# Optimization experiments

Hardware: AMD Instinct MI355X
Metric: run time of the kernel (lower is better)

Reference implementation:

```python
import jax, jax.numpy as jnp
import numpy as np

S, B, E, H, FFN = 512, 16, 512, 8, 2048
D = E // H
EPS = 1e-6
MAXT = 1.0 - 1e-7


def _norm(x):
    return jnp.sqrt(jnp.sum(x * x, axis=-1, keepdims=True) + 1e-15)


def artanh(x):
    return jnp.arctanh(jnp.clip(x, -MAXT, MAXT))


def expmap0(u):
    n = _norm(u)
    return jnp.tanh(n) * u / n


def logmap0(x):
    n = _norm(x)
    return artanh(n) * x / n


def projx(x):
    n = _norm(x)
    m = 1.0 - 1e-5
    return jnp.where(n > m, x * (m / n), x)


def lambda_x(x):
    return 2.0 / jnp.maximum(1.0 - jnp.sum(x * x, -1, keepdims=True), EPS)


def mobius_add(x, y):
    xy = jnp.sum(x * y, -1, keepdims=True)
    x2 = jnp.sum(x * x, -1, keepdims=True)
    y2 = jnp.sum(y * y, -1, keepdims=True)
    num = (1 + 2 * xy + y2) * x + (1 - x2) * y
    return num / jnp.maximum(1 + 2 * xy + x2 * y2, EPS)


def mobius_scalar_mul(r, x):
    n = _norm(x)
    return jnp.tanh(r * artanh(n)) * x / n


def mobius_matvec(W, x):
    mx = x @ W.T
    nx = _norm(x)
    nmx = _norm(mx)
    res = jnp.tanh(nmx / nx * artanh(nx)) * mx / nmx
    return jnp.where(nmx > 1e-7, res, jnp.zeros_like(mx))


def man_linear(W, b, x):
    return projx(mobius_add(mobius_matvec(W, x), expmap0(b)))


def layernorm(x, g, b):
    mu = x.mean(-1, keepdims=True)
    v = jnp.mean((x - mu) ** 2, -1, keepdims=True)
    return (x - mu) / jnp.sqrt(v + 1e-5) * g + b


def mob_res_midpoint(x1, x2):
    # two_point_mid with w1 = w2 = 1 (Mobius gyromidpoint residual)
    l1, l2 = lambda_x(x1), lambda_x(x2)
    t = (x1 * l1 + x2 * l2) / jnp.maximum(l1 + l2 - 2.0, EPS)
    return mobius_scalar_mul(0.5, t)


def _heads(t):  # [S,B,E] -> [B,H,S,D]
    return t.reshape(S, B, H, D).transpose(1, 2, 0, 3)


def _merge(t):  # [B,H,S,D] -> [S,B,E]
    return t.transpose(2, 0, 1, 3).reshape(S, B, E)


def euclid_expert(x, ln1_g, ln1_b, ln2_g, ln2_b, Wq, bq, Wk, bk, Wv, bv, Wo, bo, W1, b1, W2, b2):
    res = x
    h = layernorm(x, ln1_g, ln1_b)
    q, k, v = _heads(h @ Wq.T + bq), _heads(h @ Wk.T + bk), _heads(h @ Wv.T + bv)
    d2 = jnp.sum(q * q, -1)[..., :, None] + jnp.sum(k * k, -1)[..., None, :] - 2 * jnp.einsum('bhqd,bhkd->bhqk', q, k)
    scores = -jnp.sqrt(jnp.maximum(d2, 0.0) + 1e-12) / np.sqrt(D)
    w = jax.nn.softmax(scores, -1)
    o = _merge(jnp.einsum('bhqk,bhkd->bhqd', w, v))
    x = o @ Wo.T + bo + res
    res = x
    h = layernorm(x, ln2_g, ln2_b)
    h = jax.nn.relu(h @ W1.T + b1)
    h = jax.nn.relu(h @ W2.T + b2)
    return h + res


def hyp_expert(x, ln1_g, ln1_b, ln2_g, ln2_b, Wq, bq, Wk, bk, Wv, bv, Wo, bo, W1, b1, W2, b2):
    res = x
    h = expmap0(layernorm(logmap0(x), ln1_g, ln1_b))
    q = projx(_heads(man_linear(Wq, bq, h)))
    k = projx(_heads(man_linear(Wk, bk, h)))
    v = projx(_heads(man_linear(Wv, bv, h)))
    qq, kk = jnp.sum(q * q, -1), jnp.sum(k * k, -1)
    qk = jnp.einsum('bhqd,bhkd->bhqk', q, k)
    diff2 = jnp.maximum(qq[..., :, None] + kk[..., None, :] - 2 * qk, 0.0)
    den = jnp.maximum(1 - 2 * qk + qq[..., :, None] * kk[..., None, :], EPS)
    dist = 2.0 * artanh(jnp.sqrt(diff2 / den + 1e-15))  # Poincare dist via gyro identity
    w = jax.nn.softmax(-dist / np.sqrt(D), -1)
    lam = lambda_x(v)  # [B,H,S,1]
    num = jnp.einsum('bhqk,bhkd->bhqd', w, v * lam)
    dnm = jnp.maximum(jnp.einsum('bhqk,bhk->bhq', w, lam[..., 0] - 1.0), EPS)[..., None]
    o = projx(mobius_scalar_mul(0.5, num / dnm))  # Mobius gyromidpoint aggregation
    x = projx(man_linear(Wo, bo, projx(_merge(o))))
    x = mob_res_midpoint(x, res)
    res = x
    x = projx(expmap0(layernorm(logmap0(x), ln2_g, ln2_b)))
    x = jax.nn.relu(man_linear(W1, b1, x))
    x = jax.nn.relu(man_linear(W2, b2, x))
    return projx(mob_res_midpoint(x, res))


def setup_inputs():
    key = jax.random.key(0)
    ks = jax.random.split(key, 20)
    x0 = jax.random.normal(ks[0], (S, B, E), jnp.float32)
    x1 = projx(0.05 * jax.random.normal(ks[1], (S, B, E), jnp.float32))
    x = jnp.stack([x0, x1])

    def w(k, *shape):
        return jax.random.normal(k, (2,) + shape, jnp.float32) / np.sqrt(shape[-1])

    return dict(
        x=x,
        ln1_g=jnp.ones((2, E), jnp.float32), ln1_b=jnp.zeros((2, E), jnp.float32),
        ln2_g=jnp.ones((2, E), jnp.float32), ln2_b=jnp.zeros((2, E), jnp.float32),
        Wq=w(ks[2], E, E), bq=0.02 * jax.random.normal(ks[3], (2, E), jnp.float32),
        Wk=w(ks[4], E, E), bk=0.02 * jax.random.normal(ks[5], (2, E), jnp.float32),
        Wv=w(ks[6], E, E), bv=0.02 * jax.random.normal(ks[7], (2, E), jnp.float32),
        Wo=w(ks[8], E, E), bo=0.02 * jax.random.normal(ks[9], (2, E), jnp.float32),
        W1=w(ks[10], FFN, E), b1=0.02 * jax.random.normal(ks[11], (2, FFN), jnp.float32),
        W2=w(ks[12], E, FFN), b2=0.02 * jax.random.normal(ks[13], (2, E), jnp.float32),
    )


def reference(x, ln1_g, ln1_b, ln2_g, ln2_b, Wq, bq, Wk, bk, Wv, bv, Wo, bo, W1, b1, W2, b2):
    args = (ln1_g, ln1_b, ln2_g, ln2_b, Wq, bq, Wk, bk, Wv, bv, Wo, bo, W1, b1, W2, b2)
    out0 = euclid_expert(x[0], *[a[0] for a in args])
    out1 = hyp_expert(x[1], *[a[1] for a in args])
    return jnp.stack([out0, out1])
```

## Files before the change

### kernel.cpp

```cpp
#include <hip/hip_runtime.h>
#include <cstdint>
#include <cstddef>

#define S_ 512
#define B_ 16
#define H_ 8
#define D_ 64
#define E_ 512
#define FFN_ 2048
#define R_ (S_*B_)
#define EPSF 1e-6f
#define PROJ_M 0.99999f

typedef __attribute__((ext_vector_type(8))) short bf16x8;
typedef __attribute__((ext_vector_type(4))) float f32x4;
typedef __attribute__((ext_vector_type(2))) unsigned int u32x2;

__device__ __forceinline__ float bf2f(uint32_t u){
  union{uint32_t i; float f;} c; c.i = u<<16; return c.f;
}
__device__ __forceinline__ uint16_t f2bf(float f){
  union{float f; uint32_t i;} c; c.f = f;
  return (uint16_t)((c.i + 0x7FFFu + ((c.i>>16)&1u))>>16);
}
__device__ __forceinline__ void unpack8(uint4 u, float* f){
  f[0]=bf2f(u.x&0xFFFFu); f[1]=bf2f(u.x>>16);
  f[2]=bf2f(u.y&0xFFFFu); f[3]=bf2f(u.y>>16);
  f[4]=bf2f(u.z&0xFFFFu); f[5]=bf2f(u.z>>16);
  f[6]=bf2f(u.w&0xFFFFu); f[7]=bf2f(u.w>>16);
}
__device__ __forceinline__ uint4 pack8(const float* f){
  uint4 u;
  u.x = (uint32_t)f2bf(f[0]) | ((uint32_t)f2bf(f[1])<<16);
  u.y = (uint32_t)f2bf(f[2]) | ((uint32_t)f2bf(f[3])<<16);
  u.z = (uint32_t)f2bf(f[4]) | ((uint32_t)f2bf(f[5])<<16);
  u.w = (uint32_t)f2bf(f[6]) | ((uint32_t)f2bf(f[7])<<16);
  return u;
}
__device__ __forceinline__ float artanh_c(float x){
  return (x >= 0.99999994f) ? 8.4056215f : atanhf(x);
}
__device__ __forceinline__ float wave_sum(float x){
  #pragma unroll
  for(int o=32;o>=1;o>>=1) x += __shfl_xor(x,o);
  return x;
}
__device__ __forceinline__ float g8sum(float x){
  x += __shfl_xor(x,1); x += __shfl_xor(x,2); x += __shfl_xor(x,4);
  return x;
}
__device__ __forceinline__ float block_sum(float x, float* sb){
  x = wave_sum(x);
  const int w = threadIdx.x >> 6;
  __syncthreads();
  if((threadIdx.x & 63)==0) sb[w] = x;
  __syncthreads();
  return sb[0]+sb[1]+sb[2]+sb[3];
}
__device__ __forceinline__ void gl_lds16(const void* g, void* l){
  __builtin_amdgcn_global_load_lds(
    (const __attribute__((address_space(1))) void*)(uintptr_t)g,
    (__attribute__((address_space(3))) void*)(uint32_t)(uintptr_t)l, 16, 0, 0);
}
__device__ __forceinline__ uint32_t cvtpk(float a, float b){
  uint32_t r;
  asm("v_cvt_pk_bf16_f32 %0, %1, %2" : "=v"(r) : "v"(a), "v"(b));
  return r;
}
template<int OFF>
__device__ __forceinline__ u32x2 trrd(uint32_t addr){
  u32x2 r;
  asm volatile("ds_read_b64_tr_b16 %0, %1 offset:%2" : "=v"(r) : "v"(addr), "n"(OFF));
  return r;
}
__device__ __forceinline__ bf16x8 vcomb(u32x2 a, u32x2 b){
  union{ uint32_t u[4]; bf16x8 v; } c;
  c.u[0]=a[0]; c.u[1]=a[1]; c.u[2]=b[0]; c.u[3]=b[1];
  return c.v;
}

__global__ __launch_bounds__(256) void cvt_all(
  const float* __restrict__ Wq, const float* __restrict__ Wk,
  const float* __restrict__ Wv, const float* __restrict__ Wo,
  const float* __restrict__ W1, const float* __restrict__ W2,
  uint16_t* __restrict__ dst)
{
  int i4 = blockIdx.x*256 + threadIdx.x;
  int e = 0;
  if(i4 >= 786432){ e = 1; i4 -= 786432; }
  const int r = i4;
  const float* s;
  if(r < 65536)        s = Wq + (size_t)(r)*4        + (size_t)e*262144;
  else if(r < 131072)  s = Wk + (size_t)(r-65536)*4  + (size_t)e*262144;
  else if(r < 196608)  s = Wv + (size_t)(r-131072)*4 + (size_t)e*262144;
  else if(r < 262144)  s = Wo + (size_t)(r-196608)*4 + (size_t)e*262144;
  else if(r < 524288)  s = W1 + (size_t)(r-262144)*4 + (size_t)e*1048576;
  else                 s = W2 + (size_t)(r-524288)*4 + (size_t)e*1048576;
  const float4 f = *(const float4*)s;
  uint2 o;
  o.x = (uint32_t)f2bf(f.x) | ((uint32_t)f2bf(f.y)<<16);
  o.y = (uint32_t)f2bf(f.z) | ((uint32_t)f2bf(f.w)<<16);
  *(uint2*)(dst + (size_t)e*3145728 + (size_t)r*4) = o;
}

__global__ __launch_bounds__(256) void expmap_all(
  const float* __restrict__ bq, const float* __restrict__ bk,
  const float* __restrict__ bv, const float* __restrict__ bo,
  const float* __restrict__ b1, const float* __restrict__ b2,
  float* __restrict__ YV)
{
  __shared__ float sb[4];
  const int id = blockIdx.x, t = threadIdx.x;
  const float* src; float* dst; int C;
  if(id==0){ src=bq+E_;   dst=YV+0;    C=E_; }
  else if(id==1){ src=bk+E_;   dst=YV+528;  C=E_; }
  else if(id==2){ src=bv+E_;   dst=YV+1056; C=E_; }
  else if(id==3){ src=bo+E_;   dst=YV+1584; C=E_; }
  else if(id==4){ src=b1+FFN_; dst=YV+2112; C=FFN_; }
  else          { src=b2+E_;   dst=YV+4176; C=E_; }
  const int npc = C >> 8;
  float v[8]; float s2 = 0.f;
  for(int i=0;i<npc;i++){ v[i] = src[t+256*i]; s2 += v[i]*v[i]; }
  s2 = block_sum(s2, sb);
  const float n = sqrtf(s2 + 1e-15f);
  const float th = tanhf(n);
  const float sc = th/n;
  for(int i=0;i<npc;i++) dst[t+256*i] = v[i]*sc;
  if(t==0) dst[C] = th*th;
}

__global__ __launch_bounds__(256) void lnfuseW(const float* __restrict__ x,
  const float* __restrict__ g, const float* __restrict__ b,
  uint16_t* __restrict__ out, float* __restrict__ nout, int do_projx)
{
  const int row = blockIdx.x*4 + (threadIdx.x>>6);
  const int l = threadIdx.x & 63;
  const size_t base = (size_t)row*E_ + l*8;
  const int hyp = (row >= R_);
  const float* gg = g + (hyp? E_ : 0);
  const float* bb = b + (hyp? E_ : 0);
  float v[8];
  *(float4*)(v)   = *(const float4*)(x + base);
  *(float4*)(v+4) = *(const float4*)(x + base + 4);
  float s = 0.f;
  #pragma unroll
  for(int i=0;i<8;i++) s += v[i];
  const float mu = wave_sum(s) * (1.f/E_);
  float q = 0.f;
  #pragma unroll
  for(int i=0;i<8;i++){ v[i] -= mu; q += v[i]*v[i]; }
  const float var = wave_sum(q) * (1.f/E_);
  const float rs = 1.f/sqrtf(var + 1e-5f);
  float gv[8], bvv[8];
  *(float4*)(gv)    = *(const float4*)(gg + l*8);
  *(float4*)(gv+4)  = *(const float4*)(gg + l*8 + 4);
  *(float4*)(bvv)   = *(const float4*)(bb + l*8);
  *(float4*)(bvv+4) = *(const float4*)(bb + l*8 + 4);
  float t[8];
  #pragma unroll
  for(int i=0;i<8;i++) t[i] = v[i]*rs*gv[i] + bvv[i];
  if(hyp){
    float n = 0.f;
    #pragma unroll
    for(int i=0;i<8;i++) n += t[i]*t[i];
    n = wave_sum(n);
    const float n2 = sqrtf(n + 1e-15f);
    const float nh = tanhf(n2);
    float scl = nh/n2;
    float nrm = nh;
    if(do_projx && nrm > PROJ_M){ scl *= PROJ_M/nrm; nrm = PROJ_M; }
    #pragma unroll
    for(int i=0;i<8;i++) t[i] *= scl;
    if(l==0) nout[row - R_] = nrm;
  }
  *(uint4*)(out + base) = pack8(t);
}

__global__ __launch_bounds__(256) void qk_norms(
  const uint16_t* __restrict__ Qb, const uint16_t* __restrict__ Kb,
  float* __restrict__ qn, float* __restrict__ kn)
{
  const int w = threadIdx.x >> 6, l = threadIdx.x & 63;
  const int row = blockIdx.x*4 + w;
  const int s = row >> 4, b = row & 15;
  const size_t base = (size_t)row*E_ + l*8;
  {
    uint4 u = *(const uint4*)(Qb + base);
    float f[8]; unpack8(u, f);
    float ss = 0.f;
    #pragma unroll
    for(int i=0;i<8;i++) ss += f[i]*f[i];
    ss = g8sum(ss);
    if((l&7)==0) qn[((b<<3) + (l>>3))*512 + s] = ss;
  }
  {
    uint4 u = *(const uint4*)(Kb + base);
    float f[8]; unpack8(u, f);
    float ss = 0.f;
    #pragma unroll
    for(int i=0;i<8;i++) ss += f[i]*f[i];
    ss = g8sum(ss);
    if((l&7)==0) kn[((b<<3) + (l>>3))*512 + s] = ss;
  }
}

template<int EPL>
__global__ __launch_bounds__(256) void man_epiW(
  const uint16_t* __restrict__ mxb, const float* __restrict__ nxbuf,
  const float* __restrict__ y, uint16_t* __restrict__ outb,
  float* __restrict__ nout,
  const float* __restrict__ midres, float* __restrict__ midout, int flags)
{
  constexpr int C = EPL*64;
  const int row = blockIdx.x*4 + (threadIdx.x>>6);
  const int l = threadIdx.x & 63;
  const size_t base = (size_t)row*C + l*EPL;
  float v[EPL], yv[EPL];
  #pragma unroll
  for(int i=0;i<EPL/8;i++){
    uint4 u = *(const uint4*)(mxb + base + i*8);
    unpack8(u, v + i*8);
  }
  #pragma unroll
  for(int i=0;i<EPL/4;i++)
    *(float4*)(yv + i*4) = *(const float4*)(y + l*EPL + i*4);
  float s2 = 0.f;
  #pragma unroll
  for(int i=0;i<EPL;i++) s2 += v[i]*v[i];
  s2 = wave_sum(s2);
  const float nmx = sqrtf(s2 + 1e-15f);
  const float nx  = nxbuf[row];
  const float sc  = tanhf(nmx/nx * artanh_c(nx));
  const bool ok   = (nmx > 1e-7f);
  const float fmul = ok ? (sc/nmx) : 0.f;
  const float x2   = ok ? sc*sc : 0.f;
  float xy = 0.f;
  #pragma unroll
  for(int i=0;i<EPL;i++){ v[i] *= fmul; xy += v[i]*yv[i]; }
  xy = wave_sum(xy);
  const float y2 = y[C];
  const float aa = 1.f + 2.f*xy + y2;
  const float bb = 1.f - x2;
  const float iden = 1.f/fmaxf(1.f + 2.f*xy + x2*y2, EPSF);
  const float num2 = aa*aa*x2 + 2.f*aa*bb*xy + bb*bb*y2;
  const float nz = sqrtf(num2*iden*iden + 1e-15f);
  const float ps = (nz > PROJ_M) ? (PROJ_M/nz) : 1.f;
  float nfin = (nz > PROJ_M) ? PROJ_M : nz;
  #pragma unroll
  for(int i=0;i<EPL;i++) v[i] = (aa*v[i] + bb*yv[i]) * iden * ps;
  if(flags & 1){
    float rsu = 0.f;
    #pragma unroll
    for(int i=0;i<EPL;i++){ v[i] = fmaxf(v[i], 0.f); rsu += v[i]*v[i]; }
    rsu = wave_sum(rsu);
    nfin = sqrtf(rsu + 1e-15f);
  }
  if(midres){
    float bv2[EPL];
    #pragma unroll
    for(int i=0;i<EPL/4;i++)
      *(float4*)(bv2 + i*4) = *(const float4*)(midres + base + i*4);
    float pb = 0.f, pab = 0.f;
    #pragma unroll
    for(int i=0;i<EPL;i++){ pb += bv2[i]*bv2[i]; pab += v[i]*bv2[i]; }
    const float sa  = nfin*nfin;
    const float sbb = wave_sum(pb);
    const float sab = wave_sum(pab);
    const float l1 = 2.f/fmaxf(1.f - sa,  EPSF);
    const float l2 = 2.f/fmaxf(1.f - sbb, EPSF);
    const float idn = 1.f/fmaxf(l1 + l2 - 2.f, EPSF);
    const float nt2 = (l1*l1*sa + 2.f*l1*l2*sab + l2*l2*sbb)*idn*idn;
    const float nt = sqrtf(nt2 + 1e-15f);
    const float sfin = tanhf(0.5f*artanh_c(nt));
    float scm = sfin/nt;
    if((flags & 8) && sfin > PROJ_M) scm *= PROJ_M/sfin;
    #pragma unroll
    for(int i=0;i<EPL;i++) midout[base + i] = (v[i]*l1 + bv2[i]*l2)*idn*scm;
  } else {
    #pragma unroll
    for(int i=0;i<EPL/8;i++)
      *(uint4*)(outb + base + i*8) = pack8(v + i*8);
    if(nout && l==0) nout[row] = nfin;
  }
}

__global__ __launch_bounds__(256) void man_epi_qkvW(
  const uint16_t* __restrict__ mxb, const float* __restrict__ nxbuf,
  const float* __restrict__ YV, uint16_t* __restrict__ qkv,
  float* __restrict__ qnG, float* __restrict__ knG, float* __restrict__ lamG)
{
  const int sel = blockIdx.y;
  const int row = blockIdx.x*4 + (threadIdx.x>>6);
  const int l = threadIdx.x & 63;
  const float* y = YV + sel*528;
  const size_t base = (size_t)sel*4194304 + (size_t)row*512 + l*8;
  float v[8], yv[8];
  {
    uint4 u = *(const uint4*)(mxb + base);
    unpack8(u, v);
  }
  *(float4*)(yv)   = *(const float4*)(y + l*8);
  *(float4*)(yv+4) = *(const float4*)(y + l*8 + 4);
  float s2 = 0.f;
  #pragma unroll
  for(int i=0;i<8;i++) s2 += v[i]*v[i];
  s2 = wave_sum(s2);
  const float nmx = sqrtf(s2 + 1e-15f);
  const float nx  = nxbuf[row];
  const float sc  = tanhf(nmx/nx * artanh_c(nx));
  const bool ok   = (nmx > 1e-7f);
  const float fmul = ok ? (sc/nmx) : 0.f;
  const float x2   = ok ? sc*sc : 0.f;
  float xy = 0.f;
  #pragma unroll
  for(int i=0;i<8;i++){ v[i] *= fmul; xy += v[i]*yv[i]; }
  xy = wave_sum(xy);
  const float y2 = y[512];
  const float aa = 1.f + 2.f*xy + y2;
  const float bb = 1.f - x2;
  const float iden = 1.f/fmaxf(1.f + 2.f*xy + x2*y2, EPSF);
  const float num2 = aa*aa*x2 + 2.f*aa*bb*xy + bb*bb*y2;
  const float nz = sqrtf(num2*iden*iden + 1e-15f);
  const float ps = (nz > PROJ_M) ? (PROJ_M/nz) : 1.f;
  #pragma unroll
  for(int i=0;i<8;i++) v[i] = (aa*v[i] + bb*yv[i]) * iden * ps;
  float hs = 0.f;
  #pragma unroll
  for(int i=0;i<8;i++) hs += v[i]*v[i];
  hs = g8sum(hs);
  float nh = sqrtf(hs + 1e-15f);
  float phs = 1.f;
  if(nh > PROJ_M){ phs = PROJ_M/nh; nh = PROJ_M; }
  #pragma unroll
  for(int i=0;i<8;i++) v[i] *= phs;
  const float nh2 = nh*nh;
  const float lam = 2.f/fmaxf(1.f - nh2, EPSF);
  if(sel==2){
    #pragma unroll
    for(int i=0;i<8;i++) v[i] *= lam;
  }
  if((l & 7) == 0){
    const int s = row >> 4, b2 = row & 15;
    const int idx = ((b2<<3) + (l>>3))*512 + s;
    if(sel==0) qnG[idx] = nh2;
    else if(sel==1) knG[idx] = nh2;
    else lamG[idx] = lam;
  }
  *(uint4*)(qkv + base) = pack8(v);
}

__global__ __launch_bounds__(256) void o_finishW(const uint16_t* __restrict__ op,
  uint16_t* __restrict__ outb, float* __restrict__ nout)
{
  const int row = blockIdx.x*4 + (threadIdx.x>>6);
  const int l = threadIdx.x & 63;
  const size_t base = (size_t)row*E_ + l*8;
  float v[8];
  {
    uint4 u = *(const uint4*)(op + base);
    unpack8(u, v);
  }
  float hs = 0.f;
  #pragma unroll
  for(int i=0;i<8;i++) hs += v[i]*v[i];
  hs = g8sum(hs);
  const float ns = sqrtf(hs + 1e-15f);
  const float tt = tanhf(0.5f*artanh_c(ns));
  float scv = tt/ns;
  float sn = tt;
  if(sn > PROJ_M){ scv *= PROJ_M/sn; sn = PROJ_M; }
  float tot = 0.f;
  #pragma unroll
  for(int i=0;i<8;i++){ v[i] *= scv; tot += v[i]*v[i]; }
  tot = wave_sum(tot);
  const float n = sqrtf(tot + 1e-15f);
  float nf = n;
  if(n > PROJ_M){
    const float s = PROJ_M/n;
    #pragma unroll
    for(int i=0;i<8;i++) v[i] *= s;
    nf = PROJ_M;
  }
  *(uint4*)(outb + base) = pack8(v);
  if(l==0) nout[row] = nf;
}

__global__ __launch_bounds__(256) void gemmF(
    const uint16_t* __restrict__ A,
    const uint16_t* __restrict__ Bw0, const uint16_t* __restrict__ Bw1,
    int msplit, int N, int K, int mode0, int mode1,
    const float* __restrict__ bQ, const float* __restrict__ bK,
    const float* __restrict__ bV, const float* __restrict__ res0,
    float* __restrict__ outf0,
    uint16_t* __restrict__ outb0, uint16_t* __restrict__ outb1)
{
  __shared__ __align__(16) char AsB[2][16384];
  __shared__ __align__(16) char BsB[2][16384];
  const int gx = gridDim.x;
  int lid = blockIdx.x + gx*blockIdx.y;
  {
    const int nwg = gx*gridDim.y;
    const int cpx = nwg >> 3;
    lid = (lid & 7)*cpx + (lid >> 3);
  }
  const int m0 = (lid/gx)*128;
  const int n0 = (lid%gx)*128;
  const int e  = (m0 >= msplit);
  const uint16_t* Bw = e ? Bw1 : Bw0;
  uint16_t* ob = e ? outb1 : outb0;
  const int mode = e ? mode1 : mode0;
  const int mloc0 = m0 - (e ? msplit : 0);

  const int tid = threadIdx.x;
  const int l = tid & 63, w = tid >> 6;
  const int wm = w >> 1, wn = w & 1;
  const int lr = l & 15, g = l >> 4;
  const int lr3 = l >> 3, lc = l & 7;
  const int c8s = lc ^ lr3;
  const int swq = (lr & 7) << 4;

  const uint16_t* aSrc = A  + (size_t)(m0 + lr3)*K + c8s*8;
  const uint16_t* bSrc = Bw + (size_t)(n0 + lr3)*K + c8s*8;

  f32x4 acc[4][4];
  #pragma unroll
  for(int i=0;i<4;i++)
    #pragma unroll
    for(int j=0;j<4;j++) acc[i][j] = (f32x4){0.f,0.f,0.f,0.f};

  const int nk = K >> 6;
  #pragma unroll
  for(int c=0;c<4;c++){
    const int ci = w*4 + c;
    gl_lds16(aSrc + (size_t)(ci*8)*K, AsB[0] + ci*1024);
    gl_lds16(bSrc + (size_t)(ci*8)*K, BsB[0] + ci*1024);
  }
  for(int ks=0; ks<nk; ks++){
    __syncthreads();
    if(ks+1 < nk){
      const int k0 = (ks+1) << 6;
      #pragma unroll
      for(int c=0;c<4;c++){
        const int ci = w*4 + c;
        gl_lds16(aSrc + (size_t)(ci*8)*K + k0, AsB[(ks+1)&1] + ci*1024);
        gl_lds16(bSrc + (size_t)(ci*8)*K + k0, BsB[(ks+1)&1] + ci*1024);
      }
    }
    const char* Ac = AsB[ks&1];
    const char* Bc = BsB[ks&1];
    #pragma unroll
    for(int h=0;h<2;h++){
      bf16x8 av[4], bv[4];
      #pragma unroll
      for(int i=0;i<4;i++){
        av[i] = *(const bf16x8*)(Ac + (wm*64 + i*16 + lr)*128 + ((((h*4+g)<<4)) ^ swq));
        bv[i] = *(const bf16x8*)(Bc + (wn*64 + i*16 + lr)*128 + ((((h*4+g)<<4)) ^ swq));
      }
      #pragma unroll
      for(int i=0;i<4;i++)
        #pragma unroll
        for(int j=0;j<4;j++)
          acc[i][j] = __builtin_amdgcn_mfma_f32_16x16x32_bf16(av[i], bv[j], acc[i][j], 0,0,0);
    }
  }
  const int orow = g*4;
  #pragma unroll
  for(int i=0;i<4;i++){
    #pragma unroll
    for(int j=0;j<4;j++){
      const int gn = n0 + wn*64 + j*16 + lr;
      float bval = 0.f;
      if(mode==2||mode==3||mode==4) bval = bQ[gn];
      else if(mode==6){
        const float* bp = (gn<512)? bQ : ((gn<1024)? bK : bV);
        bval = bp[gn&511];
      }
      #pragma unroll
      for(int r=0;r<4;r++){
        const int gml = mloc0 + wm*64 + i*16 + orow + r;
        const float vv = acc[i][j][r];
        const size_t off = (size_t)gml*N + gn;
        if(mode==2){ outf0[off] = vv + bval + res0[off]; }
        else if(mode==3){ ob[off] = f2bf(fmaxf(vv + bval, 0.f)); }
        else if(mode==4){ outf0[off] = fmaxf(vv + bval, 0.f) + res0[off]; }
        else if(mode==5){ ob[off] = f2bf(vv); }
        else {
          ob[(size_t)(gn>>9)*4194304 + (size_t)gml*512 + (gn&511)] = f2bf(vv + bval);
        }
      }
    }
  }
}

__global__ __launch_bounds__(256,3) void attnF2(
  const uint16_t* __restrict__ QKV0, const uint16_t* __restrict__ QKV1,
  const float* __restrict__ qn0, const float* __restrict__ kn0,
  const float* __restrict__ qn1, const float* __restrict__ kn1,
  const float* __restrict__ lam1, uint16_t* __restrict__ OB)
{
  __shared__ __align__(16) char QsB[8192];
  __shared__ __align__(16) char KsB[2][8192];
  __shared__ __align__(16) char VtB[2][8192];
  __shared__ float kkL[512];
  __shared__ float lamL[512];

  const int tid = threadIdx.x;
  const int l = tid & 63, w = tid >> 6;
  const int lr = l & 15, g = l >> 4;
  const int lr3 = l >> 3, lc = l & 7;
  const int c8s = lc ^ lr3;
  const int swq = (lr & 7) << 4;
  int lid = blockIdx.x;
  lid = (lid & 7)*256 + (lid >> 3);
  const int hyp = lid >> 10;
  const int sub = lid & 1023;
  const int bh = sub >> 3;
  const int q0 = (sub & 7) * 64;
  const uint16_t* Qb = hyp ? QKV1 : QKV0;
  const uint16_t* Kb = Qb + 4194304;
  const uint16_t* Vb = Qb + 8388608;
  const float* qnG = hyp ? qn1 : qn0;
  const float* knG = hyp ? kn1 : kn0;
  uint16_t* outB = OB + (size_t)hyp*4194304;
  const size_t gstride = (size_t)B_*E_;
  const size_t gbase = (size_t)(bh>>3)*E_ + (size_t)(bh&7)*D_;

  int vs[2], vd[2];
  #pragma unroll
  for(int ci=0;ci<2;ci++){
    vs[ci] = (ci*8 + (l>>3))*4 + ((l>>1)&3);
    vd[ci] = w*16 + (l&1)*8;
  }

  #pragma unroll
  for(int c=0;c<2;c++){
    const int ci = w*2 + c;
    gl_lds16(Qb + (size_t)(q0 + ci*8 + lr3)*gstride + gbase + c8s*8, QsB + ci*1024);
    gl_lds16(Kb + (size_t)(ci*8 + lr3)*gstride + gbase + c8s*8, KsB[0] + ci*1024);
    gl_lds16(Vb + (size_t)vs[c]*gstride + gbase + vd[c], VtB[0] + w*2048 + c*1024);
  }
  kkL[tid]       = knG[bh*512 + tid];
  kkL[tid + 256] = knG[bh*512 + 256 + tid];
  if(hyp){
    lamL[tid]       = lam1[bh*512 + tid];
    lamL[tid + 256] = lam1[bh*512 + 256 + tid];
  }
  __syncthreads();

  const int qrow = w*16 + lr;
  bf16x8 qf0, qf1;
  qf0 = *(const bf16x8*)(QsB + qrow*128 + ((g<<4) ^ swq));
  qf1 = *(const bf16x8*)(QsB + qrow*128 + (((4+g)<<4) ^ swq));
  const float qq = qnG[bh*512 + q0 + qrow];

  f32x4 oa[4];
  #pragma unroll
  for(int m=0;m<4;m++) oa[m] = (f32x4){0.f,0.f,0.f,0.f};
  float lrun = 0.f, dnr = 0.f;

  const uint32_t vaddr_base = (uint32_t)(uintptr_t)(&VtB[0][0]) + (uint32_t)(l*8);

  for(int kt=0; kt<8; kt++){
    if(kt < 7){
      #pragma unroll
      for(int c=0;c<2;c++){
        const int ci = w*2 + c;
        gl_lds16(Kb + (size_t)((kt+1)*64 + ci*8 + lr3)*gstride + gbase + c8s*8,
                 KsB[(kt+1)&1] + ci*1024);
        gl_lds16(Vb + (size_t)((kt+1)*64 + vs[c])*gstride + gbase + vd[c],
                 VtB[(kt+1)&1] + w*2048 + c*1024);
      }
    }
    const char* Kc = KsB[kt&1];
    const float* kkt = &kkL[kt*64];
    const float* lmt = &lamL[kt*64];

    f32x4 st[4];
    #pragma unroll
    for(int t=0;t<4;t++){
      const bf16x8 ka0 = *(const bf16x8*)(Kc + (t*16+lr)*128 + ((g<<4) ^ swq));
      const bf16x8 ka1 = *(const bf16x8*)(Kc + (t*16+lr)*128 + (((4+g)<<4) ^ swq));
      f32x4 c0 = (f32x4){0.f,0.f,0.f,0.f};
      c0 = __builtin_amdgcn_mfma_f32_16x16x32_bf16(ka0, qf0, c0, 0,0,0);
      c0 = __builtin_amdgcn_mfma_f32_16x16x32_bf16(ka1, qf1, c0, 0,0,0);
      st[t] = c0;
    }

    uint32_t pbw[8];
    {
      float ls = 0.f, dl = 0.f;
      #pragma unroll
      for(int t=0;t<4;t++){
        const f32x4 kkv = *(const f32x4*)(kkt + t*16 + g*4);
        float p[4];
        #pragma unroll
        for(int r=0;r<4;r++){
          const float qk = st[t][r], kk = kkv[r];
          const float a = qq + kk;
          if(hyp){
            const float u = fmaxf(fmaf(-2.f, qk, a), 0.f);
            const float v = fmaxf(fmaf(qq, kk, fmaf(-2.f, qk, 1.f)), EPSF);
            const float wz = __builtin_amdgcn_sqrtf(u*v);
            const float den = (u + v) + 2.f*wz;
            float ratio = (v - u) * __builtin_amdgcn_rcpf(den);
            ratio = fmaxf(ratio, 5.9604645e-8f);
            p[r] = __builtin_amdgcn_exp2f(0.125f * __builtin_amdgcn_logf(ratio));
          } else {
            const float d2 = fmaxf(fmaf(-2.f, qk, a), 0.f) + 1e-12f;
            p[r] = __builtin_amdgcn_exp2f(-0.18033688f * __builtin_amdgcn_sqrtf(d2));
          }
        }
        ls += (p[0]+p[1])+(p[2]+p[3]);
        if(hyp){
          const f32x4 lv = *(const f32x4*)(lmt + t*16 + g*4);
          dl += p[0]*(lv[0]-1.f) + p[1]*(lv[1]-1.f) + p[2]*(lv[2]-1.f) + p[3]*(lv[3]-1.f);
        }
        pbw[t*2]   = cvtpk(p[0], p[1]);
        pbw[t*2+1] = cvtpk(p[2], p[3]);
      }
      ls += __shfl_xor(ls,16); ls += __shfl_xor(ls,32);
      lrun += ls;
      if(hyp){
        dl += __shfl_xor(dl,16); dl += __shfl_xor(dl,32);
        dnr += dl;
      }
    }

    const uint32_t va_kt = vaddr_base + (uint32_t)((kt&1)*8192);
    {
      u32x2 r00=trrd<0>(va_kt),    r01=trrd<512>(va_kt);
      u32x2 r10=trrd<2048>(va_kt), r11=trrd<2560>(va_kt);
      u32x2 r20=trrd<4096>(va_kt), r21=trrd<4608>(va_kt);
      u32x2 r30=trrd<6144>(va_kt), r31=trrd<6656>(va_kt);
      asm volatile("s_waitcnt lgkmcnt(0)" ::: "memory");
      __builtin_amdgcn_sched_barrier(0);
      bf16x8 pb0;
      { union{uint32_t u[4]; bf16x8 v;} c;
        c.u[0]=pbw[0]; c.u[1]=pbw[1]; c.u[2]=pbw[2]; c.u[3]=pbw[3]; pb0=c.v; }
      __builtin_amdgcn_s_setprio(1);
      oa[0] = __builtin_amdgcn_mfma_f32_16x16x32_bf16(vcomb(r00,r01), pb0, oa[0], 0,0,0);
      oa[1] = __builtin_amdgcn_mfma_f32_16x16x32_bf16(vcomb(r10,r11), pb0, oa[1], 0,0,0);
      oa[2] = __builtin_amdgcn_mfma_f32_16x16x32_bf16(vcomb(r20,r21), pb0, oa[2], 0,0,0);
      oa[3] = __builtin_amdgcn_mfma_f32_16x16x32_bf16(vcomb(r30,r31), pb0, oa[3], 0,0,0);
      __builtin_amdgcn_s_setprio(0);
    }
    {
      u32x2 r00=trrd<1024>(va_kt), r01=trrd<1536>(va_kt);
      u32x2 r10=trrd<3072>(va_kt), r11=trrd<3584>(va_kt);
      u32x2 r20=trrd<5120>(va_kt), r21=trrd<5632>(va_kt);
      u32x2 r30=trrd<7168>(va_kt), r31=trrd<7680>(va_kt);
      asm volatile("s_waitcnt lgkmcnt(0)" ::: "memory");
      __builtin_amdgcn_sched_barrier(0);
      bf16x8 pb0;
      { union{uint32_t u[4]; bf16x8 v;} c;
        c.u[0]=pbw[4]; c.u[1]=pbw[5]; c.u[2]=pbw[6]; c.u[3]=pbw[7]; pb0=c.v; }
      __builtin_amdgcn_s_setprio(1);
      oa[0] = __builtin_amdgcn_mfma_f32_16x16x32_bf16(vcomb(r00,r01), pb0, oa[0], 0,0,0);
      oa[1] = __builtin_amdgcn_mfma_f32_16x16x32_bf16(vcomb(r10,r11), pb0, oa[1], 0,0,0);
      oa[2] = __builtin_amdgcn_mfma_f32_16x16x32_bf16(vcomb(r20,r21), pb0, oa[2], 0,0,0);
      oa[3] = __builtin_amdgcn_mfma_f32_16x16x32_bf16(vcomb(r30,r31), pb0, oa[3], 0,0,0);
      __builtin_amdgcn_s_setprio(0);
    }
    __syncthreads();
  }

  char* OTB = (char*)KsB;
  float scale;
  {
    const float invl = 1.f/lrun;
    if(hyp){
      const float dn = fmaxf(dnr*invl, EPSF);
      scale = invl/dn;
    } else scale = invl;
  }
  #pragma unroll
  for(int m=0;m<4;m++){
    f32x4 vv;
    vv[0]=oa[m][0]*scale; vv[1]=oa[m][1]*scale;
    vv[2]=oa[m][2]*scale; vv[3]=oa[m][3]*scale;
    *(f32x4*)(OTB + w*4096 + lr*256 + ((m*64 + g*16) ^ ((lr&7)<<4))) = vv;
  }
  __syncthreads();
  {
    const int row = tid >> 2, cw = tid & 3;
    const int wsrc = row >> 4, ql = row & 15;
    float vals[16];
    #pragma unroll
    for(int ii=0;ii<4;ii++)
      *(f32x4*)&vals[ii*4] = *(const f32x4*)(OTB + wsrc*4096 + ql*256 + ((cw*64 + ii*16) ^ ((ql&7)<<4)));
    const size_t go = (size_t)(q0 + row)*gstride + gbase + cw*16;
    *(uint4*)(outB + go)     = pack8(vals);
    *(uint4*)(outB + go + 8) = pack8(vals+8);
  }
}

extern "C" void kernel_launch(void* const* d_in, const int* in_sizes, int n_in,
                              void* d_out, int out_size, void* d_ws, size_t ws_size,
                              hipStream_t stream)
{
  (void)in_sizes; (void)n_in; (void)out_size; (void)ws_size;
  const float* x    = (const float*)d_in[0];
  const float* ln1g = (const float*)d_in[1];
  const float* ln1b = (const float*)d_in[2];
  const float* ln2g = (const float*)d_in[3];
  const float* ln2b = (const float*)d_in[4];
  const float* Wq = (const float*)d_in[5];
  const float* bq = (const float*)d_in[6];
  const float* Wk = (const float*)d_in[7];
  const float* bk = (const float*)d_in[8];
  const float* Wv = (const float*)d_in[9];
  const float* bv = (const float*)d_in[10];
  const float* Wo = (const float*)d_in[11];
  const float* bo = (const float*)d_in[12];
  const float* W1 = (const float*)d_in[13];
  const float* b1 = (const float*)d_in[14];
  const float* W2 = (const float*)d_in[15];
  const float* b2 = (const float*)d_in[16];
  float* out = (float*)d_out;
  const float* x1 = x + (size_t)R_*E_;

  char* ws = (char*)d_ws;
  uint16_t* HB   = (uint16_t*)(ws);
  uint16_t* F1B  = (uint16_t*)(ws + ((size_t)16<<20));
  uint16_t* QKV0 = (uint16_t*)(ws + ((size_t)16<<20));
  uint16_t* QKV1 = (uint16_t*)(ws + ((size_t)40<<20));
  uint16_t* OB   = (uint16_t*)(ws + ((size_t)64<<20));
  float*    X2   = (float*)   (ws + ((size_t)80<<20));
  float*    X2e1 = X2 + (size_t)R_*E_;
  uint16_t* WB   = (uint16_t*)(ws + ((size_t)112<<20));
  char*     aux  = ws + ((size_t)124<<20);
  float*    YV   = (float*)(aux);
  float*    NH   = (float*)(aux + (32<<10));
  float*    NO   = NH + R_;
  float*    N3   = NO + R_;
  float*    N4   = N3 + R_;
  float*    qn0  = (float*)(aux + (256<<10));
  float*    kn0  = qn0 + 65536;
  float*    qn1  = kn0 + 65536;
  float*    kn1  = qn1 + 65536;
  float*    lam1 = kn1 + 65536;

  uint16_t* WBe = WB + 3145728;

  cvt_all<<<6144,256,0,stream>>>(Wq,Wk,Wv,Wo,W1,W2, WB);
  expmap_all<<<6,256,0,stream>>>(bq,bk,bv,bo,b1,b2, YV);

  lnfuseW<<<4096,256,0,stream>>>(x, ln1g, ln1b, HB, NH, 0);

  gemmF<<<dim3(12,128),256,0,stream>>>(HB, WB, WBe, R_, 1536, 512, 6, 7,
                                       bq, bk, bv, nullptr, nullptr, QKV0, QKV1);
  qk_norms<<<2048,256,0,stream>>>(QKV0, QKV0+4194304, qn0, kn0);
  man_epi_qkvW<<<dim3(2048,3),256,0,stream>>>(QKV1, NH, YV, QKV1, qn1, kn1, lam1);

  attnF2<<<2048,256,0,stream>>>(QKV0, QKV1, qn0, kn0, qn1, kn1, lam1, OB);
  o_finishW<<<2048,256,0,stream>>>(OB + (size_t)R_*E_, OB + (size_t)R_*E_, NO);

  gemmF<<<dim3(4,128),256,0,stream>>>(OB, WB+786432, WBe+786432, R_, 512, 512, 2, 5,
                                      bo, nullptr, nullptr, x, X2, nullptr, HB);
  man_epiW<8><<<2048,256,0,stream>>>(HB, NO, YV+1584, nullptr, nullptr, x1, X2e1, 0);

  lnfuseW<<<4096,256,0,stream>>>(X2, ln2g, ln2b, HB, N3, 1);

  gemmF<<<dim3(16,128),256,0,stream>>>(HB, WB+1048576, WBe+1048576, R_, 2048, 512, 3, 5,
                                       b1, nullptr, nullptr, nullptr, nullptr,
                                       F1B, F1B + (size_t)R_*FFN_);
  man_epiW<32><<<2048,256,0,stream>>>(F1B + (size_t)R_*FFN_, N3, YV+2112,
                                      F1B + (size_t)R_*FFN_, N4, nullptr, nullptr, 1);

  gemmF<<<dim3(4,128),256,0,stream>>>(F1B, WB+2097152, WBe+2097152, R_, 512, 2048, 4, 5,
                                      b2, nullptr, nullptr, X2, out, nullptr, HB);
  man_epiW<8><<<2048,256,0,stream>>>(HB, N4, YV+4176, nullptr, nullptr,
                                     X2e1, out + (size_t)R_*E_, 1|8);
}
```

Before: 393.9 us.

## Shrink GEMM K-tile to cut LDS use and stage epilogue through shared memory

The GEMM K step drops from 64 to 32, which halves the double-buffered LDS footprint, and launch bounds now request 4 waves per SIMD so more workgroups can be resident. The epilogue writes accumulators into padded shared memory and then emits coalesced float4 and packed 8×bf16 stores, replacing scattered scalar stores. The QKV split mode now selects the bias and output pointer once per block. The tradeoffs are twice as many barriers and K iterations, extra barriers in the epilogue, and possible register spilling under the tighter occupancy bound.

Result: faster. 373.6 us (-5.1%).

```diff
diff --git a/kernel.cpp b/kernel.cpp
--- a/kernel.cpp
+++ b/kernel.cpp
@@ -385,7 +385,7 @@
   if(l==0) nout[row] = nf;
 }
 
-__global__ __launch_bounds__(256) void gemmF(
+__global__ __launch_bounds__(256,4) void gemmF(
     const uint16_t* __restrict__ A,
     const uint16_t* __restrict__ Bw0, const uint16_t* __restrict__ Bw1,
     int msplit, int N, int K, int mode0, int mode1,
@@ -394,8 +394,7 @@
     float* __restrict__ outf0,
     uint16_t* __restrict__ outb0, uint16_t* __restrict__ outb1)
 {
-  __shared__ __align__(16) char AsB[2][16384];
-  __shared__ __align__(16) char BsB[2][16384];
+  __shared__ __align__(16) char smem[33792];
   const int gx = gridDim.x;
   int lid = blockIdx.x + gx*blockIdx.y;
   {
@@ -415,12 +414,12 @@
   const int l = tid & 63, w = tid >> 6;
   const int wm = w >> 1, wn = w & 1;
   const int lr = l & 15, g = l >> 4;
-  const int lr3 = l >> 3, lc = l & 7;
-  const int c8s = lc ^ lr3;
-  const int swq = (lr & 7) << 4;
-
-  const uint16_t* aSrc = A  + (size_t)(m0 + lr3)*K + c8s*8;
-  const uint16_t* bSrc = Bw + (size_t)(n0 + lr3)*K + c8s*8;
+
+  const int srow4 = l >> 2;
+  const int schunk = ((l & 3) ^ ((l >> 3) & 3)) << 3;
+  const uint16_t* aS = A  + (size_t)(m0 + w*32 + srow4)*K + schunk;
+  const uint16_t* bS = Bw + (size_t)(n0 + w*32 + srow4)*K + schunk;
+  const int posq = (g ^ ((lr >> 1) & 3)) << 4;
 
   f32x4 acc[4][4];
   #pragma unroll
@@ -428,65 +427,109 @@
     #pragma unroll
     for(int j=0;j<4;j++) acc[i][j] = (f32x4){0.f,0.f,0.f,0.f};
 
-  const int nk = K >> 6;
-  #pragma unroll
-  for(int c=0;c<4;c++){
-    const int ci = w*4 + c;
-    gl_lds16(aSrc + (size_t)(ci*8)*K, AsB[0] + ci*1024);
-    gl_lds16(bSrc + (size_t)(ci*8)*K, BsB[0] + ci*1024);
-  }
+  const int nk = K >> 5;
+
+#define STG(ks, b) { \
+    const int k0_ = (ks) << 5; \
+    char* ad_ = smem + (b)*8192 + w*2048; \
+    char* bd_ = smem + 16384 + (b)*8192 + w*2048; \
+    gl_lds16(aS + k0_,                 ad_); \
+    gl_lds16(aS + (size_t)16*K + k0_,  ad_ + 1024); \
+    gl_lds16(bS + k0_,                 bd_); \
+    gl_lds16(bS + (size_t)16*K + k0_,  bd_ + 1024); \
+  }
+
+  STG(0, 0);
   for(int ks=0; ks<nk; ks++){
     __syncthreads();
-    if(ks+1 < nk){
-      const int k0 = (ks+1) << 6;
+    if(ks+1 < nk) STG(ks+1, (ks+1)&1);
+    const char* Ac = smem + (ks&1)*8192;
+    const char* Bc = smem + 16384 + (ks&1)*8192;
+    bf16x8 av[4], bv[4];
+    #pragma unroll
+    for(int i=0;i<4;i++){
+      av[i] = *(const bf16x8*)(Ac + (wm*64 + i*16 + lr)*64 + posq);
+      bv[i] = *(const bf16x8*)(Bc + (wn*64 + i*16 + lr)*64 + posq);
+    }
+    #pragma unroll
+    for(int i=0;i<4;i++)
       #pragma unroll
-      for(int c=0;c<4;c++){
-        const int ci = w*4 + c;
-        gl_lds16(aSrc + (size_t)(ci*8)*K + k0, AsB[(ks+1)&1] + ci*1024);
-        gl_lds16(bSrc + (size_t)(ci*8)*K + k0, BsB[(ks+1)&1] + ci*1024);
+      for(int j=0;j<4;j++)
+        acc[i][j] = __builtin_amdgcn_mfma_f32_16x16x32_bf16(av[i], bv[j], acc[i][j], 0,0,0);
+  }
+#undef STG
+
+  float* Ep = (float*)smem;
+  const int ecr = tid >> 2;
+  const int ecb = (tid & 3) * 32;
+  const float* bptr = bQ;
+  uint16_t* obase = ob;
+  int ncol0 = n0;
+  size_t ostride = (size_t)N;
+  if(mode==6 || mode==7){
+    const int sel = n0 >> 9;
+    obase = ob + (size_t)sel*4194304;
+    ncol0 = n0 & 511;
+    ostride = 512;
+    if(mode==6) bptr = (sel==0)? bQ : ((sel==1)? bK : bV);
+  }
+  #pragma unroll
+  for(int p=0;p<2;p++){
+    __syncthreads();
+    #pragma unroll
+    for(int i2=0;i2<2;i2++){
+      const int i = p*2 + i2;
+      const int cr = wm*32 + i2*16 + g*4;
+      #pragma unroll
+      for(int j=0;j<4;j++){
+        const int col = wn*64 + j*16 + lr;
+        Ep[(cr+0)*132 + col] = acc[i][j][0];
+        Ep[(cr+1)*132 + col] = acc[i][j][1];
+        Ep[(cr+2)*132 + col] = acc[i][j][2];
+        Ep[(cr+3)*132 + col] = acc[i][j][3];
       }
     }
-    const char* Ac = AsB[ks&1];
-    const char* Bc = BsB[ks&1];
-    #pragma unroll
-    for(int h=0;h<2;h++){
-      bf16x8 av[4], bv[4];
+    __syncthreads();
+    const int grow = mloc0 + (ecr & 31) + ((ecr >> 5) << 6) + p*32;
+    const float* Er = Ep + ecr*132 + ecb;
+    if(mode==2 || mode==4){
       #pragma unroll
-      for(int i=0;i<4;i++){
-        av[i] = *(const bf16x8*)(Ac + (wm*64 + i*16 + lr)*128 + ((((h*4+g)<<4)) ^ swq));
-        bv[i] = *(const bf16x8*)(Bc + (wn*64 + i*16 + lr)*128 + ((((h*4+g)<<4)) ^ swq));
+      for(int k=0;k<8;k++){
+        const int colg = n0 + ecb + k*4;
+        float4 vv = *(const float4*)(Er + k*4);
+        const float4 bb4 = *(const float4*)(bQ + colg);
+        const size_t off = (size_t)grow*N + colg;
+        const float4 rr4 = *(const float4*)(res0 + off);
+        float4 o4;
+        if(mode==2){
+          o4.x = vv.x + bb4.x + rr4.x; o4.y = vv.y + bb4.y + rr4.y;
+          o4.z = vv.z + bb4.z + rr4.z; o4.w = vv.w + bb4.w + rr4.w;
+        } else {
+          o4.x = fmaxf(vv.x + bb4.x, 0.f) + rr4.x; o4.y = fmaxf(vv.y + bb4.y, 0.f) + rr4.y;
+          o4.z = fmaxf(vv.z + bb4.z, 0.f) + rr4.z; o4.w = fmaxf(vv.w + bb4.w, 0.f) + rr4.w;
+        }
+        *(float4*)(outf0 + off) = o4;
       }
+    } else {
       #pragma unroll
-      for(int i=0;i<4;i++)
-        #pragma unroll
-        for(int j=0;j<4;j++)
-          acc[i][j] = __builtin_amdgcn_mfma_f32_16x16x32_bf16(av[i], bv[j], acc[i][j], 0,0,0);
-    }
-  }
-  const int orow = g*4;
-  #pragma unroll
-  for(int i=0;i<4;i++){
-    #pragma unroll
-    for(int j=0;j<4;j++){
-      const int gn = n0 + wn*64 + j*16 + lr;
-      float bval = 0.f;
-      if(mode==2||mode==3||mode==4) bval = bQ[gn];
-      else if(mode==6){
-        const float* bp = (gn<512)? bQ : ((gn<1024)? bK : bV);
-        bval = bp[gn&511];
-      }
-      #pragma unroll
-      for(int r=0;r<4;r++){
-        const int gml = mloc0 + wm*64 + i*16 + orow + r;
-        const float vv = acc[i][j][r];
-        const size_t off = (size_t)gml*N + gn;
-        if(mode==2){ outf0[off] = vv + bval + res0[off]; }
-        else if(mode==3){ ob[off] = f2bf(fmaxf(vv + bval, 0.f)); }
-        else if(mode==4){ outf0[off] = fmaxf(vv + bval, 0.f) + res0[off]; }
-        else if(mode==5){ ob[off] = f2bf(vv); }
-        else {
-          ob[(size_t)(gn>>9)*4194304 + (size_t)gml*512 + (gn&511)] = f2bf(vv + bval);
+      for(int k=0;k<4;k++){
+        const int colact = ecb + k*8;
+        float f[8];
+        *(float4*)(f)   = *(const float4*)(Er + k*8);
+        *(float4*)(f+4) = *(const float4*)(Er + k*8 + 4);
+        if(mode==3 || mode==6){
+          float bb8[8];
+          *(float4*)(bb8)   = *(const float4*)(bptr + ncol0 + colact);
+          *(float4*)(bb8+4) = *(const float4*)(bptr + ncol0 + colact + 4);
+          if(mode==3){
+            #pragma unroll
+            for(int i=0;i<8;i++) f[i] = fmaxf(f[i] + bb8[i], 0.f);
+          } else {
+            #pragma unroll
+            for(int i=0;i<8;i++) f[i] = f[i] + bb8[i];
+          }
         }
+        *(uint4*)(obase + (size_t)grow*ostride + ncol0 + colact) = pack8(f);
       }
     }
   }
```
